# Performance work log

Hardware: AMD Instinct MI355X
Metric: run time of the kernel (lower is better)

The kernel has to match this reference:

```python
import jax, jax.numpy as jnp
import numpy as np

B, S, D, DI = 8, 4096, 512, 2048
EPS = 1e-12  # torch F.normalize eps


def _l2norm(x):
    n = jnp.sqrt(jnp.sum(x * x, axis=-1, keepdims=True))
    return x / jnp.maximum(n, EPS)


def setup_inputs() -> dict:
    key = jax.random.key(0)
    ks = jax.random.split(key, 10)
    sd = 1.0 / np.sqrt(D)
    si = 1.0 / np.sqrt(DI)
    return {
        "x": jax.random.normal(ks[0], (B, S, D), jnp.float32),
        "wq": jax.random.uniform(ks[1], (D, DI), jnp.float32, -sd, sd),
        "wk": jax.random.uniform(ks[2], (D, DI), jnp.float32, -sd, sd),
        "wv": jax.random.uniform(ks[3], (D, DI), jnp.float32, -sd, sd),
        "wo": jax.random.uniform(ks[4], (DI, D), jnp.float32, -si, si),
        "w1": jax.random.uniform(ks[5], (D, DI), jnp.float32, -sd, sd),
        "b1": jax.random.uniform(ks[6], (DI,), jnp.float32, -sd, sd),
        "w2": jax.random.uniform(ks[7], (DI, D), jnp.float32, -si, si),
        "b2": jax.random.uniform(ks[8], (D,), jnp.float32, -si, si),
    }


def reference(x, wq, wk, wv, wo, w1, b1, w2, b2):
    # Hydra attention (linear): normalize(q) * sum_s(normalize(k)*v)
    q = _l2norm(jnp.einsum('bsd,de->bse', x, wq))
    k = _l2norm(jnp.einsum('bsd,de->bse', x, wk))
    v = jnp.einsum('bsd,de->bse', x, wv)
    kv = jnp.sum(k * v, axis=-2, keepdims=True)  # [B,1,DI]
    attn = jnp.einsum('bse,ed->bsd', q * kv, wo) + x  # dropout = identity (eval)
    # position-wise FFN with residual
    h = jax.nn.relu(jnp.einsum('bsd,de->bse', attn, w1) + b1)
    out = jnp.einsum('bse,ed->bsd', h, w2) + b2 + attn
    return out
```

## Files before the change

### kernel.cpp

```cpp
#include <hip/hip_runtime.h>
#include <stdint.h>

#define Bb  8
#define Ss  4096
#define Dd  512
#define DIi 2048
#define Mm  (Bb*Ss)

typedef unsigned short u16;
typedef __bf16 bf16x8 __attribute__((ext_vector_type(8)));
typedef float  f32x4  __attribute__((ext_vector_type(4)));

__device__ __forceinline__ float bfu(unsigned int u) {
  return __uint_as_float((u & 0xffffu) << 16);
}
__device__ __forceinline__ u16 f2bu(float f) {
  unsigned int x = __float_as_uint(f);
  return (u16)((x + 0x7fffu + ((x >> 16) & 1u)) >> 16);
}

__device__ __forceinline__ void tr_tile(const float* __restrict__ W, u16* __restrict__ Wt,
                                        int K, int N, int local, int tid) {
  __shared__ float t[32][33];
  const int nx = N / 32;
  const int n0 = (local % nx) * 32, k0 = (local / nx) * 32;
  const int tx = tid & 31, ty = tid >> 5;
#pragma unroll
  for (int i = 0; i < 32; i += 8)
    t[ty + i][tx] = W[(long)(k0 + ty + i) * N + n0 + tx];
  __syncthreads();
#pragma unroll
  for (int i = 0; i < 32; i += 8)
    Wt[(long)(n0 + ty + i) * K + k0 + tx] = f2bu(t[tx][ty + i]);
}

__global__ __launch_bounds__(256) void prep(
    const float* __restrict__ x, u16* __restrict__ xb,
    const float* wv, const float* w1, const float* wo, const float* w2,
    const float* wq, const float* wk,
    u16* wvT, u16* w1T, u16* woT, u16* w2T, u16* wqb, u16* wkb,
    float* __restrict__ zptr) {
  const int bid = blockIdx.x, tid = threadIdx.x;
  if (bid < 320) {
    zptr[bid * 256 + tid] = 0.f;
  } else if (bid < 2368) {
    long i = (long)(bid - 320) * 256 + tid;
    const long n4 = (long)Mm * Dd / 4;
    const long st = 2048L * 256;
    for (; i < n4; i += st) {
      float4 v = ((const float4*)x)[i];
      ushort4 o;
      o.x = f2bu(v.x); o.y = f2bu(v.y); o.z = f2bu(v.z); o.w = f2bu(v.w);
      ((ushort4*)xb)[i] = o;
    }
  } else if (bid < 3392)  tr_tile(wv, wvT, Dd, DIi, bid - 2368, tid);
  else if (bid < 4416)    tr_tile(w1, w1T, Dd, DIi, bid - 3392, tid);
  else if (bid < 5440)    tr_tile(wo, woT, DIi, Dd, bid - 4416, tid);
  else if (bid < 6464)    tr_tile(w2, w2T, DIi, Dd, bid - 5440, tid);
  else if (bid < 7488) {
    long i = (long)(bid - 6464) * 256 + tid;
    float4 v = ((const float4*)wq)[i];
    ushort4 o;
    o.x = f2bu(v.x); o.y = f2bu(v.y); o.z = f2bu(v.z); o.w = f2bu(v.w);
    ((ushort4*)wqb)[i] = o;
  } else {
    long i = (long)(bid - 7488) * 256 + tid;
    float4 v = ((const float4*)wk)[i];
    ushort4 o;
    o.x = f2bu(v.x); o.y = f2bu(v.y); o.z = f2bu(v.z); o.w = f2bu(v.w);
    ((ushort4*)wkb)[i] = o;
  }
}

__global__ __launch_bounds__(256) void build_wob(const u16* __restrict__ woT,
                                                 const float* __restrict__ kv,
                                                 u16* __restrict__ wob) {
  const int b = blockIdx.y;
  long i = (long)blockIdx.x * 256 + threadIdx.x;
  const long tot = (long)Dd * DIi / 8;
  if (i >= tot) return;
  const long e = i * 8;
  const int k = (int)(e & (DIi - 1));
  ushort4 w0 = *(const ushort4*)(woT + e);
  ushort4 w1 = *(const ushort4*)(woT + e + 4);
  const float* kvp = kv + (long)b * DIi + k;
  ushort4 o0, o1;
  o0.x = f2bu(bfu(w0.x) * kvp[0]); o0.y = f2bu(bfu(w0.y) * kvp[1]);
  o0.z = f2bu(bfu(w0.z) * kvp[2]); o0.w = f2bu(bfu(w0.w) * kvp[3]);
  o1.x = f2bu(bfu(w1.x) * kvp[4]); o1.y = f2bu(bfu(w1.y) * kvp[5]);
  o1.z = f2bu(bfu(w1.z) * kvp[6]); o1.w = f2bu(bfu(w1.w) * kvp[7]);
  u16* dst = wob + (long)b * Dd * DIi + e;
  *(ushort4*)dst = o0;
  *(ushort4*)(dst + 4) = o1;
}

__global__ void tr_x(const u16* __restrict__ xb, const float* __restrict__ nksq,
                     u16* __restrict__ xT, u16* __restrict__ xrnT) {
  __shared__ u16 t[32][33];
  __shared__ float rns[32];
  const int b = blockIdx.z;
  const int s0 = blockIdx.y * 32, d0 = blockIdx.x * 32;
  const int tx = threadIdx.x, ty = threadIdx.y;
  const size_t sbase = (size_t)b * Ss + s0;
#pragma unroll
  for (int i = 0; i < 32; i += 8)
    t[ty + i][tx] = xb[(sbase + ty + i) * Dd + d0 + tx];
  if (ty == 0) {
    const float nk = fmaxf(nksq[sbase + tx], 0.f);
    rns[tx] = 1.f / fmaxf(sqrtf(nk), 1e-12f);
  }
  __syncthreads();
  const size_t dbase = (size_t)b * Dd + d0;
#pragma unroll
  for (int i = 0; i < 32; i += 8) {
    const u16 v = t[tx][ty + i];
    const size_t idx = (dbase + ty + i) * Ss + s0 + tx;
    xT[idx] = v;
    xrnT[idx] = f2bu(bfu(v) * rns[tx]);
  }
}

__global__ __launch_bounds__(256) void colsum_kv(const u16* __restrict__ wkb,
                                                 const u16* __restrict__ Tb,
                                                 float* __restrict__ kv) {
  const int b = blockIdx.y;
  const int e = blockIdx.x * 256 + threadIdx.x;
  const int d0 = blockIdx.z * 64;
  const u16* wp = wkb + (size_t)d0 * DIi + e;
  const u16* tp = Tb + (size_t)b * Dd * DIi + (size_t)d0 * DIi + e;
  float a = 0.f;
#pragma unroll 4
  for (int d = 0; d < 64; ++d) {
    a += bfu(wp[0]) * bfu(tp[0]);
    wp += DIi; tp += DIi;
  }
  atomicAdd(&kv[(size_t)b * DIi + e], a);
}

#define GLL(src, dst) \
  __builtin_amdgcn_global_load_lds((const __attribute__((address_space(1))) unsigned int*)(src), \
                                   (__attribute__((address_space(3))) unsigned int*)(dst), 16, 0, 0)

enum { G_FFN1 = 2, G_FFN2 = 3 };

template<int MODE>
__global__ __launch_bounds__(512, 2) void gemm8(
    const u16* __restrict__ A, const u16* __restrict__ Bt,
    int N, int K,
    u16* __restrict__ Ybf, float* __restrict__ Yf,
    const u16* __restrict__ resb, const float* __restrict__ bias)
{
  __shared__ u16 lds8[65536];

  const int nxg = gridDim.x;
  const int s = blockIdx.y * nxg + blockIdx.x;
  const int xcd = s & 7, j = s >> 3;
  const int by = xcd * (gridDim.y >> 3) + j / nxg;
  const int bx = j % nxg;

  const int tid  = threadIdx.x;
  const int lane = tid & 63;
  const int wid  = tid >> 6;
  const int wr = wid >> 2, wc = wid & 3;
  const int l15 = lane & 15, lg = lane >> 4;

  const long bm0 = (long)by * 256;
  const long bn0 = (long)bx * 256;
  const int NT = K >> 6;

  const u16* pA = A + bm0 * K;
  const u16* pB = Bt + bn0 * K;

  const int rowT = ((tid >> 6) << 3) | (tid & 7);
  const int cc8  = ((tid >> 3) & 7) * 8;

#define STAGE(PTR, LD, H, TT, BUFU, REGU) do {                                  \
    const u16* s0_ = (PTR) + (size_t)((H) * 128 + rowT) * (LD)                  \
                     + (size_t)(TT) * 64 + cc8;                                 \
    u16* d_ = lds8 + (BUFU) + (REGU) + (H) * 8192 + wid * 512;                  \
    GLL(s0_, d_);                                                               \
    GLL(s0_ + (size_t)64 * (LD), d_ + 4096);                                    \
  } while (0)

  const int aoff = (wr * 16384 + (l15 >> 3) * 1024 + lg * 128 + (l15 & 7) * 16) >> 1;
  const int boff = (32768 + (wc >> 1) * 16384 + (wc & 1) * 8192 +
                    (l15 >> 3) * 1024 + lg * 128 + (l15 & 7) * 16) >> 1;
#define LDA(M_, KS_, BU_) (*(const bf16x8*)(lds8 + (BU_) + aoff + (M_) * 1024 + (KS_) * 256))
#define LDB(N_, KS_, BU_) (*(const bf16x8*)(lds8 + (BU_) + boff + (N_) * 1024 + (KS_) * 256))

  f32x4 acc[8][4] = {};

  STAGE(pA, K, 0, 0, 0, 0);
  STAGE(pA, K, 1, 0, 0, 0);
  STAGE(pB, K, 0, 0, 0, 16384);
  STAGE(pB, K, 1, 0, 0, 16384);
  STAGE(pA, K, 0, 1, 32768, 0);
  asm volatile("s_waitcnt vmcnt(2)" ::: "memory");
  __builtin_amdgcn_s_barrier();

  for (int t = 0; t < NT; ++t) {
    const int bufu = (t & 1) * 32768;
    const int nbuf = bufu ^ 32768;
    bf16x8 aF[4], bF[4];

#pragma unroll
    for (int n = 0; n < 4; ++n) bF[n] = LDB(n, 0, bufu);
#pragma unroll
    for (int m = 0; m < 4; ++m) aF[m] = LDA(m, 0, bufu);
    if (t + 1 < NT) STAGE(pA, K, 1, t + 1, nbuf, 0);
    __builtin_amdgcn_s_barrier();
    __builtin_amdgcn_s_setprio(1);
#pragma unroll
    for (int m = 0; m < 4; ++m)
#pragma unroll
      for (int n = 0; n < 4; ++n)
        acc[m][n] = __builtin_amdgcn_mfma_f32_16x16x32_bf16(aF[m], bF[n], acc[m][n], 0, 0, 0);
    __builtin_amdgcn_s_setprio(0);

#pragma unroll
    for (int m = 0; m < 4; ++m) aF[m] = LDA(4 + m, 0, bufu);
    if (t + 1 < NT) STAGE(pB, K, 0, t + 1, nbuf, 16384);
    __builtin_amdgcn_s_barrier();
    __builtin_amdgcn_s_setprio(1);
#pragma unroll
    for (int m = 0; m < 4; ++m)
#pragma unroll
      for (int n = 0; n < 4; ++n)
        acc[4 + m][n] = __builtin_amdgcn_mfma_f32_16x16x32_bf16(aF[m], bF[n], acc[4 + m][n], 0, 0, 0);
    __builtin_amdgcn_s_setprio(0);

#pragma unroll
    for (int n = 0; n < 4; ++n) bF[n] = LDB(n, 1, bufu);
#pragma unroll
    for (int m = 0; m < 4; ++m) aF[m] = LDA(m, 1, bufu);
    if (t + 1 < NT) STAGE(pB, K, 1, t + 1, nbuf, 16384);
    __builtin_amdgcn_s_barrier();
    __builtin_amdgcn_s_setprio(1);
#pragma unroll
    for (int m = 0; m < 4; ++m)
#pragma unroll
      for (int n = 0; n < 4; ++n)
        acc[m][n] = __builtin_amdgcn_mfma_f32_16x16x32_bf16(aF[m], bF[n], acc[m][n], 0, 0, 0);
    __builtin_amdgcn_s_setprio(0);

#pragma unroll
    for (int m = 0; m < 4; ++m) aF[m] = LDA(4 + m, 1, bufu);
    __builtin_amdgcn_s_barrier();
    __builtin_amdgcn_s_setprio(1);
#pragma unroll
    for (int m = 0; m < 4; ++m)
#pragma unroll
      for (int n = 0; n < 4; ++n)
        acc[4 + m][n] = __builtin_amdgcn_mfma_f32_16x16x32_bf16(aF[m], bF[n], acc[4 + m][n], 0, 0, 0);
    __builtin_amdgcn_s_setprio(0);

    if (t + 1 < NT) {
      __builtin_amdgcn_s_barrier();
      if (t + 2 < NT) {
        STAGE(pA, K, 0, t + 2, bufu, 0);
        asm volatile("s_waitcnt vmcnt(2)" ::: "memory");
      } else {
        asm volatile("s_waitcnt vmcnt(0)" ::: "memory");
      }
      __builtin_amdgcn_s_barrier();
    }
  }

#pragma unroll
  for (int m = 0; m < 8; ++m) {
    const long row0 = bm0 + wr * 128 + m * 16 + lg * 4;
#pragma unroll
    for (int n = 0; n < 4; ++n) {
      const long col = bn0 + wc * 64 + n * 16 + l15;
#pragma unroll
      for (int r = 0; r < 4; ++r) {
        const long idx = (row0 + r) * N + col;
        const float v = acc[m][n][r];
        if constexpr (MODE == G_FFN1) {
          float o = v + bias[col];
          o = o > 0.f ? o : 0.f;
          Ybf[idx] = f2bu(o);
        } else {
          Yf[idx] = v + bias[col] + bfu(resb[idx]);
        }
      }
    }
  }
#undef STAGE
#undef LDA
#undef LDB
}

__global__ __launch_bounds__(256) void mega64t(
    const u16* __restrict__ wqb, const u16* __restrict__ wkb,
    const u16* __restrict__ wob,
    u16* __restrict__ Gt, u16* __restrict__ Gkt, u16* __restrict__ Ut, int zbase)
{
  __shared__ u16 As[2048];
  __shared__ u16 Bs[2048];
  const int K = DIi;
  const int idx = blockIdx.z + zbase;
  const u16* A  = (idx == 1) ? wkb : wqb;
  const u16* Bt = (idx == 0) ? wqb : (idx == 1) ? wkb
                  : wob + (size_t)(idx - 2) * Dd * DIi;
  u16* Ct = (idx == 0) ? Gt : (idx == 1) ? Gkt
            : Ut + (size_t)(idx - 2) * Dd * Dd;

  const int tid = threadIdx.x, lane = tid & 63, w = tid >> 6;
  const int wr = w >> 1, wc = w & 1;
  const int l15 = lane & 15, lg = lane >> 4;
  const long bm0 = (long)blockIdx.y * 64;
  const long bn0 = (long)blockIdx.x * 64;

  const u16* aS0 = A  + (bm0 + (tid >> 2)) * K + (tid & 3) * 8;
  const u16* bS0 = Bt + (bn0 + (tid >> 2)) * K + (tid & 3) * 8;
  u16* aD0 = As + w * 512;
  u16* bD0 = Bs + w * 512;

  f32x4 acc[2][2] = {};

  for (int k0 = 0; k0 < K; k0 += 32) {
    GLL(aS0 + k0, aD0);
    GLL(bS0 + k0, bD0);
    __syncthreads();
    bf16x8 af[2], bfv[2];
#pragma unroll
    for (int m = 0; m < 2; ++m)
      af[m] = *(const bf16x8*)(As + (wr * 32 + m * 16 + l15) * 32 + lg * 8);
#pragma unroll
    for (int n = 0; n < 2; ++n)
      bfv[n] = *(const bf16x8*)(Bs + (wc * 32 + n * 16 + l15) * 32 + lg * 8);
#pragma unroll
    for (int m = 0; m < 2; ++m)
#pragma unroll
      for (int n = 0; n < 2; ++n)
        acc[m][n] = __builtin_amdgcn_mfma_f32_16x16x32_bf16(af[m], bfv[n], acc[m][n], 0, 0, 0);
    __syncthreads();
  }

#pragma unroll
  for (int m = 0; m < 2; ++m) {
    const int row0 = (int)bm0 + wr * 32 + m * 16 + lg * 4;
#pragma unroll
    for (int n = 0; n < 2; ++n) {
      const int col = (int)bn0 + wc * 32 + n * 16 + l15;
      ushort4 o;
      o.x = f2bu(acc[m][n][0]); o.y = f2bu(acc[m][n][1]);
      o.z = f2bu(acc[m][n][2]); o.w = f2bu(acc[m][n][3]);
      *(ushort4*)(Ct + (size_t)col * Dd + row0) = o;
    }
  }
}

__global__ __launch_bounds__(256) void megacb(
    const u16* __restrict__ xrnT, const u16* __restrict__ xT,
    u16* __restrict__ Cb)
{
  __shared__ u16 As[2048];
  __shared__ u16 Bs[2048];
  const int K = Ss;
  const int z = blockIdx.z;
  const u16* A  = xrnT + (size_t)z * Dd * Ss;
  const u16* Bt = xT   + (size_t)z * Dd * Ss;
  u16* C = Cb + (size_t)z * Dd * Dd;

  const int s = blockIdx.y * 8 + blockIdx.x;
  const int byR = s & 7;
  const int bxR = s >> 3;

  const int tid = threadIdx.x, lane = tid & 63, w = tid >> 6;
  const int wr = w >> 1, wc = w & 1;
  const int l15 = lane & 15, lg = lane >> 4;
  const long bm0 = (long)byR * 64;
  const long bn0 = (long)bxR * 64;

  const u16* aS0 = A  + (bm0 + (tid >> 2)) * K + (tid & 3) * 8;
  const u16* bS0 = Bt + (bn0 + (tid >> 2)) * K + (tid & 3) * 8;
  u16* aD0 = As + w * 512;
  u16* bD0 = Bs + w * 512;

  f32x4 acc[2][2] = {};

  for (int k0 = 0; k0 < K; k0 += 32) {
    GLL(aS0 + k0, aD0);
    GLL(bS0 + k0, bD0);
    __syncthreads();
    bf16x8 af[2], bfv[2];
#pragma unroll
    for (int m = 0; m < 2; ++m)
      af[m] = *(const bf16x8*)(As + (wr * 32 + m * 16 + l15) * 32 + lg * 8);
#pragma unroll
    for (int n = 0; n < 2; ++n)
      bfv[n] = *(const bf16x8*)(Bs + (wc * 32 + n * 16 + l15) * 32 + lg * 8);
#pragma unroll
    for (int m = 0; m < 2; ++m)
#pragma unroll
      for (int n = 0; n < 2; ++n)
        acc[m][n] = __builtin_amdgcn_mfma_f32_16x16x32_bf16(af[m], bfv[n], acc[m][n], 0, 0, 0);
    __syncthreads();
  }

#pragma unroll
  for (int m = 0; m < 2; ++m) {
    const long row0 = bm0 + wr * 32 + m * 16 + lg * 4;
#pragma unroll
    for (int n = 0; n < 2; ++n) {
      const long col = bn0 + wc * 32 + n * 16 + l15;
#pragma unroll
      for (int r = 0; r < 4; ++r)
        C[(row0 + r) * Dd + col] = f2bu(acc[m][n][r]);
    }
  }
}

__global__ __launch_bounds__(256) void megatb(
    const u16* __restrict__ Cb, const u16* __restrict__ wvT,
    u16* __restrict__ Tb)
{
  __shared__ u16 As[4096];
  __shared__ u16 Bs[4096];
  const int K = Dd, N = DIi;
  const int z = blockIdx.z;
  const u16* A  = Cb + (size_t)z * Dd * Dd;
  u16* C = Tb + (size_t)z * Dd * DIi;

  const int tid = threadIdx.x, lane = tid & 63, w = tid >> 6;
  const int wr = w >> 1, wc = w & 1;
  const int l15 = lane & 15, lg = lane >> 4;
  const long bm0 = (long)blockIdx.y * 128;
  const long bn0 = (long)blockIdx.x * 128;

  const int c0 = tid, c1 = tid + 256;
  const u16* aS0 = A   + (bm0 + (c0 >> 2)) * K + (c0 & 3) * 8;
  const u16* aS1 = A   + (bm0 + (c1 >> 2)) * K + (c1 & 3) * 8;
  const u16* bS0 = wvT + (bn0 + (c0 >> 2)) * K + (c0 & 3) * 8;
  const u16* bS1 = wvT + (bn0 + (c1 >> 2)) * K + (c1 & 3) * 8;
  u16* aD0 = As + w * 512;
  u16* aD1 = As + 2048 + w * 512;
  u16* bD0 = Bs + w * 512;
  u16* bD1 = Bs + 2048 + w * 512;

  f32x4 acc[4][4] = {};

  for (int k0 = 0; k0 < K; k0 += 32) {
    GLL(aS0 + k0, aD0);
    GLL(aS1 + k0, aD1);
    GLL(bS0 + k0, bD0);
    GLL(bS1 + k0, bD1);
    __syncthreads();
    bf16x8 af[4], bfv[4];
#pragma unroll
    for (int m = 0; m < 4; ++m)
      af[m] = *(const bf16x8*)(As + (wr * 64 + m * 16 + l15) * 32 + lg * 8);
#pragma unroll
    for (int n = 0; n < 4; ++n)
      bfv[n] = *(const bf16x8*)(Bs + (wc * 64 + n * 16 + l15) * 32 + lg * 8);
#pragma unroll
    for (int m = 0; m < 4; ++m)
#pragma unroll
      for (int n = 0; n < 4; ++n)
        acc[m][n] = __builtin_amdgcn_mfma_f32_16x16x32_bf16(af[m], bfv[n], acc[m][n], 0, 0, 0);
    __syncthreads();
  }

#pragma unroll
  for (int m = 0; m < 4; ++m) {
    const long row0 = bm0 + wr * 64 + m * 16 + lg * 4;
#pragma unroll
    for (int n = 0; n < 4; ++n) {
      const long col = bn0 + wc * 64 + n * 16 + l15;
#pragma unroll
      for (int r = 0; r < 4; ++r)
        C[(row0 + r) * N + col] = f2bu(acc[m][n][r]);
    }
  }
}

template<int MODE>
__global__ __launch_bounds__(256) void mega_nx(
    const u16* __restrict__ xb, const u16* __restrict__ Gt, const u16* __restrict__ Gkt,
    const u16* __restrict__ Ut,
    float* __restrict__ nqsq, float* __restrict__ nksq, u16* __restrict__ attnb)
{
  __shared__ u16 As[4096];
  __shared__ u16 Bs[4096];
  __shared__ u16 xs[16384];
  const int K = Dd, N = Dd;

  const int nxg = gridDim.x;
  const int sId = blockIdx.y * nxg + blockIdx.x;
  const int xcd = sId & 7, jId = sId >> 3;
  const int byR = xcd * (gridDim.y >> 3) + jId / nxg;
  const int bxR = jId % nxg;

  const int tid = threadIdx.x, lane = tid & 63, w = tid >> 6;
  const int wr = w >> 1, wc = w & 1;
  const int l15 = lane & 15, lg = lane >> 4;
  const bool isK = (MODE == 0) && (byR >= Mm / 128);
  const long bm0 = (long)(isK ? byR - Mm / 128 : byR) * 128;
  const long bn0 = (long)bxR * 128;
  const int bq = (int)(bm0 >> 12);
  const u16* Bt = (MODE == 0) ? (isK ? Gkt : Gt) : Ut + (size_t)bq * Dd * Dd;
  float* nsq = (MODE == 0) ? (isK ? nksq : nqsq) : nqsq;

  const int c0 = tid, c1 = tid + 256;
  const u16* aS0 = xb + (bm0 + (c0 >> 2)) * K + (c0 & 3) * 8;
  const u16* aS1 = xb + (bm0 + (c1 >> 2)) * K + (c1 & 3) * 8;
  const u16* bS0 = Bt + (bn0 + (c0 >> 2)) * K + (c0 & 3) * 8;
  const u16* bS1 = Bt + (bn0 + (c1 >> 2)) * K + (c1 & 3) * 8;
  u16* aD0 = As + w * 512;
  u16* aD1 = As + 2048 + w * 512;
  u16* bD0 = Bs + w * 512;
  u16* bD1 = Bs + 2048 + w * 512;

  f32x4 acc[4][4] = {};

  for (int k0 = 0; k0 < K; k0 += 32) {
    GLL(aS0 + k0, aD0);
    GLL(aS1 + k0, aD1);
    GLL(bS0 + k0, bD0);
    GLL(bS1 + k0, bD1);
    __syncthreads();
    bf16x8 af[4], bfv[4];
#pragma unroll
    for (int m = 0; m < 4; ++m)
      af[m] = *(const bf16x8*)(As + (wr * 64 + m * 16 + l15) * 32 + lg * 8);
#pragma unroll
    for (int n = 0; n < 4; ++n)
      bfv[n] = *(const bf16x8*)(Bs + (wc * 64 + n * 16 + l15) * 32 + lg * 8);
#pragma unroll
    for (int m = 0; m < 4; ++m)
#pragma unroll
      for (int n = 0; n < 4; ++n)
        acc[m][n] = __builtin_amdgcn_mfma_f32_16x16x32_bf16(af[m], bfv[n], acc[m][n], 0, 0, 0);
    __syncthreads();
  }

#pragma unroll
  for (int i = 0; i < 8; ++i) {
    const int c = i * 256 + tid;
    const int rowL = c >> 4;
    const int srcslot = (c & 15) ^ (rowL & 15);
    const u16* src = xb + (size_t)(bm0 + rowL) * Dd + bn0 + srcslot * 8;
    GLL(src, xs + i * 2048 + w * 512);
  }
  asm volatile("s_waitcnt vmcnt(0)" ::: "memory");
  __builtin_amdgcn_s_barrier();

#define XV(RL, CL) bfu(xs[(RL) * 128 + ((((CL) >> 3) ^ ((RL) & 15)) << 3) + ((CL) & 7)])

  if constexpr (MODE == 0) {
    float sk[16];
#pragma unroll
    for (int i = 0; i < 16; ++i) sk[i] = 0.f;
#pragma unroll
    for (int m = 0; m < 4; ++m) {
#pragma unroll
      for (int n = 0; n < 4; ++n) {
        const int colL = wc * 64 + n * 16 + l15;
#pragma unroll
        for (int r = 0; r < 4; ++r) {
          const int rowL = wr * 64 + m * 16 + lg * 4 + r;
          sk[m * 4 + r] += acc[m][n][r] * XV(rowL, colL);
        }
      }
    }
#pragma unroll
    for (int i = 0; i < 16; ++i) {
#pragma unroll
      for (int off = 1; off < 16; off <<= 1)
        sk[i] += __shfl_xor(sk[i], off, 64);
    }
    if (l15 == 0) {
#pragma unroll
      for (int m = 0; m < 4; ++m)
#pragma unroll
        for (int r = 0; r < 4; ++r)
          atomicAdd(&nsq[bm0 + wr * 64 + m * 16 + lg * 4 + r], sk[m * 4 + r]);
    }
  } else {
#pragma unroll
    for (int m = 0; m < 4; ++m) {
      const long row0 = bm0 + wr * 64 + m * 16 + lg * 4;
      float rq[4];
#pragma unroll
      for (int r = 0; r < 4; ++r)
        rq[r] = 1.f / fmaxf(sqrtf(fmaxf(nqsq[row0 + r], 0.f)), 1e-12f);
#pragma unroll
      for (int n = 0; n < 4; ++n) {
        const int colL = wc * 64 + n * 16 + l15;
#pragma unroll
        for (int r = 0; r < 4; ++r) {
          const int rowL = wr * 64 + m * 16 + lg * 4 + r;
          attnb[(row0 + r) * N + bn0 + colL] = f2bu(acc[m][n][r] * rq[r] + XV(rowL, colL));
        }
      }
    }
  }
#undef XV
}

extern "C" void kernel_launch(void* const* d_in, const int* in_sizes, int n_in,
                              void* d_out, int out_size, void* d_ws, size_t ws_size,
                              hipStream_t stream) {
  const float* x  = (const float*)d_in[0];
  const float* wq = (const float*)d_in[1];
  const float* wk = (const float*)d_in[2];
  const float* wv = (const float*)d_in[3];
  const float* wo = (const float*)d_in[4];
  const float* w1 = (const float*)d_in[5];
  const float* b1 = (const float*)d_in[6];
  const float* w2 = (const float*)d_in[7];
  const float* b2 = (const float*)d_in[8];
  float* out = (float*)d_out;

  char* p = (char*)d_ws;
  auto take = [&](size_t bytes) {
    char* r = p; p += (bytes + 255) & ~(size_t)255; return r;
  };
  u16*   xb    = (u16*)take((size_t)Mm * Dd * 2);
  u16*   wvT   = (u16*)take((size_t)DIi * Dd * 2);
  u16*   w1T   = (u16*)take((size_t)DIi * Dd * 2);
  u16*   woT   = (u16*)take((size_t)Dd * DIi * 2);
  u16*   w2T   = (u16*)take((size_t)Dd * DIi * 2);
  u16*   wqb   = (u16*)take((size_t)Dd * DIi * 2);
  u16*   wkb   = (u16*)take((size_t)Dd * DIi * 2);
  u16*   Gt    = (u16*)take((size_t)Dd * Dd * 2);
  u16*   Gkt   = (u16*)take((size_t)Dd * Dd * 2);
  u16*   Ut    = (u16*)take((size_t)Bb * Dd * Dd * 2);
  u16*   buf1  = (u16*)take((size_t)Mm * DIi * 2);
  u16*   attnb = (u16*)take((size_t)Mm * Dd * 2);
  float* nksq  = (float*)take((size_t)Mm * 4);
  float* nqsq  = (float*)take((size_t)Mm * 4);
  float* kvp   = (float*)take((size_t)Bb * DIi * 4);
  u16* xT   = buf1;
  u16* xrnT = buf1 + (size_t)Mm * Dd;
  u16* Tb   = buf1 + 2 * (size_t)Mm * Dd;
  u16* Cb   = buf1 + 2 * (size_t)Mm * Dd + (size_t)Bb * Dd * DIi;
  u16* wob  = buf1 + 2 * (size_t)Mm * Dd + (size_t)Bb * Dd * DIi
                   + (size_t)Bb * Dd * Dd;
  (void)in_sizes; (void)n_in; (void)out_size; (void)ws_size;

  prep<<<8512, 256, 0, stream>>>(x, xb, wv, w1, wo, w2, wq, wk,
                                 wvT, w1T, woT, w2T, wqb, wkb, nksq);

  mega64t<<<dim3(8, 8, 2), 256, 0, stream>>>(wqb, wkb, nullptr, Gt, Gkt, Ut, 0);

  mega_nx<0><<<dim3(4, 2 * Mm / 128), 256, 0, stream>>>(
      xb, Gt, Gkt, nullptr, nqsq, nksq, nullptr);

  tr_x<<<dim3(Dd / 32, Ss / 32, Bb), dim3(32, 8), 0, stream>>>(xb, nksq, xT, xrnT);

  megacb<<<dim3(8, 8, Bb), 256, 0, stream>>>(xrnT, xT, Cb);

  megatb<<<dim3(16, 4, Bb), 256, 0, stream>>>(Cb, wvT, Tb);

  colsum_kv<<<dim3(8, Bb, 8), 256, 0, stream>>>(wkb, Tb, kvp);

  build_wob<<<dim3(512, Bb), 256, 0, stream>>>(woT, kvp, wob);

  mega64t<<<dim3(8, 8, 8), 256, 0, stream>>>(wqb, wkb, wob, Gt, Gkt, Ut, 2);

  mega_nx<1><<<dim3(4, Mm / 128), 256, 0, stream>>>(
      xb, nullptr, nullptr, Ut, nqsq, nullptr, attnb);

  gemm8<G_FFN1><<<dim3(DIi / 256, Mm / 256), 512, 0, stream>>>(
      attnb, w1T, DIi, Dd, buf1, nullptr, nullptr, b1);

  gemm8<G_FFN2><<<dim3(Dd / 256, Mm / 256), 512, 0, stream>>>(
      buf1, w2T, Dd, DIi, nullptr, out, attnb, b2);
}
```

Baseline: 448.6 us.

## Fuse kv column-sum into megatb epilogue and kv scaling into mega64t

```diff
diff --git a/kernel.cpp b/kernel.cpp
--- a/kernel.cpp
+++ b/kernel.cpp
@@ -72,28 +72,6 @@
   }
 }
 
-__global__ __launch_bounds__(256) void build_wob(const u16* __restrict__ woT,
-                                                 const float* __restrict__ kv,
-                                                 u16* __restrict__ wob) {
-  const int b = blockIdx.y;
-  long i = (long)blockIdx.x * 256 + threadIdx.x;
-  const long tot = (long)Dd * DIi / 8;
-  if (i >= tot) return;
-  const long e = i * 8;
-  const int k = (int)(e & (DIi - 1));
-  ushort4 w0 = *(const ushort4*)(woT + e);
-  ushort4 w1 = *(const ushort4*)(woT + e + 4);
-  const float* kvp = kv + (long)b * DIi + k;
-  ushort4 o0, o1;
-  o0.x = f2bu(bfu(w0.x) * kvp[0]); o0.y = f2bu(bfu(w0.y) * kvp[1]);
-  o0.z = f2bu(bfu(w0.z) * kvp[2]); o0.w = f2bu(bfu(w0.w) * kvp[3]);
-  o1.x = f2bu(bfu(w1.x) * kvp[4]); o1.y = f2bu(bfu(w1.y) * kvp[5]);
-  o1.z = f2bu(bfu(w1.z) * kvp[6]); o1.w = f2bu(bfu(w1.w) * kvp[7]);
-  u16* dst = wob + (long)b * Dd * DIi + e;
-  *(ushort4*)dst = o0;
-  *(ushort4*)(dst + 4) = o1;
-}
-
 __global__ void tr_x(const u16* __restrict__ xb, const float* __restrict__ nksq,
                      u16* __restrict__ xT, u16* __restrict__ xrnT) {
   __shared__ u16 t[32][33];
@@ -118,23 +96,6 @@
     xT[idx] = v;
     xrnT[idx] = f2bu(bfu(v) * rns[tx]);
   }
-}
-
-__global__ __launch_bounds__(256) void colsum_kv(const u16* __restrict__ wkb,
-                                                 const u16* __restrict__ Tb,
-                                                 float* __restrict__ kv) {
-  const int b = blockIdx.y;
-  const int e = blockIdx.x * 256 + threadIdx.x;
-  const int d0 = blockIdx.z * 64;
-  const u16* wp = wkb + (size_t)d0 * DIi + e;
-  const u16* tp = Tb + (size_t)b * Dd * DIi + (size_t)d0 * DIi + e;
-  float a = 0.f;
-#pragma unroll 4
-  for (int d = 0; d < 64; ++d) {
-    a += bfu(wp[0]) * bfu(tp[0]);
-    wp += DIi; tp += DIi;
-  }
-  atomicAdd(&kv[(size_t)b * DIi + e], a);
 }
 
 #define GLL(src, dst) \
@@ -293,18 +254,19 @@
 
 __global__ __launch_bounds__(256) void mega64t(
     const u16* __restrict__ wqb, const u16* __restrict__ wkb,
-    const u16* __restrict__ wob,
+    const u16* __restrict__ woT, const float* __restrict__ kv,
     u16* __restrict__ Gt, u16* __restrict__ Gkt, u16* __restrict__ Ut, int zbase)
 {
   __shared__ u16 As[2048];
   __shared__ u16 Bs[2048];
   const int K = DIi;
   const int idx = blockIdx.z + zbase;
+  const bool scaleB = (idx >= 2);
   const u16* A  = (idx == 1) ? wkb : wqb;
-  const u16* Bt = (idx == 0) ? wqb : (idx == 1) ? wkb
-                  : wob + (size_t)(idx - 2) * Dd * DIi;
+  const u16* Bt = (idx == 0) ? wqb : (idx == 1) ? wkb : woT;
   u16* Ct = (idx == 0) ? Gt : (idx == 1) ? Gkt
             : Ut + (size_t)(idx - 2) * Dd * Dd;
+  const float* kvb = scaleB ? (kv + (size_t)(idx - 2) * DIi) : nullptr;
 
   const int tid = threadIdx.x, lane = tid & 63, w = tid >> 6;
   const int wr = w >> 1, wc = w & 1;
@@ -330,6 +292,18 @@
 #pragma unroll
     for (int n = 0; n < 2; ++n)
       bfv[n] = *(const bf16x8*)(Bs + (wc * 32 + n * 16 + l15) * 32 + lg * 8);
+    if (scaleB) {
+      const float* kp = kvb + k0 + lg * 8;
+      float kvv[8];
+#pragma unroll
+      for (int j = 0; j < 8; ++j) kvv[j] = kp[j];
+#pragma unroll
+      for (int n = 0; n < 2; ++n) {
+        u16* bp = (u16*)&bfv[n];
+#pragma unroll
+        for (int j = 0; j < 8; ++j) bp[j] = f2bu(bfu(bp[j]) * kvv[j]);
+      }
+    }
 #pragma unroll
     for (int m = 0; m < 2; ++m)
 #pragma unroll
@@ -415,14 +389,13 @@
 
 __global__ __launch_bounds__(256) void megatb(
     const u16* __restrict__ Cb, const u16* __restrict__ wvT,
-    u16* __restrict__ Tb)
+    const u16* __restrict__ wkb, float* __restrict__ kv)
 {
   __shared__ u16 As[4096];
   __shared__ u16 Bs[4096];
-  const int K = Dd, N = DIi;
+  const int K = Dd;
   const int z = blockIdx.z;
-  const u16* A  = Cb + (size_t)z * Dd * Dd;
-  u16* C = Tb + (size_t)z * Dd * DIi;
+  const u16* A = Cb + (size_t)z * Dd * Dd;
 
   const int tid = threadIdx.x, lane = tid & 63, w = tid >> 6;
   const int wr = w >> 1, wc = w & 1;
@@ -463,15 +436,28 @@
     __syncthreads();
   }
 
+  float cs[4] = {0.f, 0.f, 0.f, 0.f};
 #pragma unroll
   for (int m = 0; m < 4; ++m) {
-    const long row0 = bm0 + wr * 64 + m * 16 + lg * 4;
+    const long drow0 = bm0 + wr * 64 + m * 16 + lg * 4;
 #pragma unroll
     for (int n = 0; n < 4; ++n) {
       const long col = bn0 + wc * 64 + n * 16 + l15;
 #pragma unroll
       for (int r = 0; r < 4; ++r)
-        C[(row0 + r) * N + col] = f2bu(acc[m][n][r]);
+        cs[n] += bfu(wkb[(drow0 + r) * DIi + col]) * acc[m][n][r];
+    }
+  }
+#pragma unroll
+  for (int n = 0; n < 4; ++n) {
+    cs[n] += __shfl_xor(cs[n], 16, 64);
+    cs[n] += __shfl_xor(cs[n], 32, 64);
+  }
+  if (lane < 16) {
+#pragma unroll
+    for (int n = 0; n < 4; ++n) {
+      const long col = bn0 + wc * 64 + n * 16 + l15;
+      atomicAdd(&kv[(size_t)z * DIi + col], cs[n]);
     }
   }
 }
@@ -635,16 +621,14 @@
   float* kvp   = (float*)take((size_t)Bb * DIi * 4);
   u16* xT   = buf1;
   u16* xrnT = buf1 + (size_t)Mm * Dd;
-  u16* Tb   = buf1 + 2 * (size_t)Mm * Dd;
-  u16* Cb   = buf1 + 2 * (size_t)Mm * Dd + (size_t)Bb * Dd * DIi;
-  u16* wob  = buf1 + 2 * (size_t)Mm * Dd + (size_t)Bb * Dd * DIi
-                   + (size_t)Bb * Dd * Dd;
+  u16* Cb   = buf1 + 2 * (size_t)Mm * Dd;
   (void)in_sizes; (void)n_in; (void)out_size; (void)ws_size;
 
   prep<<<8512, 256, 0, stream>>>(x, xb, wv, w1, wo, w2, wq, wk,
                                  wvT, w1T, woT, w2T, wqb, wkb, nksq);
 
-  mega64t<<<dim3(8, 8, 2), 256, 0, stream>>>(wqb, wkb, nullptr, Gt, Gkt, Ut, 0);
+  mega64t<<<dim3(8, 8, 2), 256, 0, stream>>>(
+      wqb, wkb, woT, kvp, Gt, Gkt, Ut, 0);
 
   mega_nx<0><<<dim3(4, 2 * Mm / 128), 256, 0, stream>>>(
       xb, Gt, Gkt, nullptr, nqsq, nksq, nullptr);
@@ -653,13 +637,10 @@
 
   megacb<<<dim3(8, 8, Bb), 256, 0, stream>>>(xrnT, xT, Cb);
 
-  megatb<<<dim3(16, 4, Bb), 256, 0, stream>>>(Cb, wvT, Tb);
-
-  colsum_kv<<<dim3(8, Bb, 8), 256, 0, stream>>>(wkb, Tb, kvp);
-
-  build_wob<<<dim3(512, Bb), 256, 0, stream>>>(woT, kvp, wob);
-
-  mega64t<<<dim3(8, 8, 8), 256, 0, stream>>>(wqb, wkb, wob, Gt, Gkt, Ut, 2);
+  megatb<<<dim3(16, 4, Bb), 256, 0, stream>>>(Cb, wvT, wkb, kvp);
+
+  mega64t<<<dim3(8, 8, 8), 256, 0, stream>>>(
+      wqb, wkb, woT, kvp, Gt, Gkt, Ut, 2);
 
   mega_nx<1><<<dim3(4, Mm / 128), 256, 0, stream>>>(
       xb, nullptr, nullptr, Ut, nqsq, nullptr, attnb);
```

Measured after the change: 452.2 us. Within noise of the previous version (+0.8%).
